# Kernel optimization log

Measured on AMD Instinct MI355X. Metric: run time of the kernel, lower is better.

The kernel has to match this reference:

```python
import jax, jax.numpy as jnp
import numpy as np

D_MODEL = 1024
N_HEADS = 16
HEAD_DIM = D_MODEL // N_HEADS
NUM_SINK = 4
WINDOW = 512
B, S = 1, 4096


def _sink_visible(S):
    # visible[i, j] = (j <= i) & ((j < NUM_SINK) | (j >= i - WINDOW + 1))
    i = jnp.arange(S)[:, None]
    j = jnp.arange(S)[None, :]
    return (j <= i) & ((j < NUM_SINK) | (j >= i - WINDOW + 1))


def setup_inputs() -> dict:
    key = jax.random.key(0)
    kx, kq, kk, kv, ko = jax.random.split(key, 5)
    sc = 1.0 / np.sqrt(D_MODEL)
    return {
        "x": jax.random.normal(kx, (B, S, D_MODEL), dtype=jnp.float32),
        "Wq": jax.random.normal(kq, (D_MODEL, D_MODEL), dtype=jnp.float32) * sc,
        "Wk": jax.random.normal(kk, (D_MODEL, D_MODEL), dtype=jnp.float32) * sc,
        "Wv": jax.random.normal(kv, (D_MODEL, D_MODEL), dtype=jnp.float32) * sc,
        "Wo": jax.random.normal(ko, (D_MODEL, D_MODEL), dtype=jnp.float32) * sc,
    }


def reference(x, Wq, Wk, Wv, Wo):
    Bx, Sx, D = x.shape
    H, hd = N_HEADS, HEAD_DIM
    # nn.Linear (no bias): y = x @ W^T
    q = (x @ Wq.T).reshape(Bx, Sx, H, hd).transpose(0, 2, 1, 3)  # (B,H,S,hd)
    k = (x @ Wk.T).reshape(Bx, Sx, H, hd).transpose(0, 2, 1, 3)
    v = (x @ Wv.T).reshape(Bx, Sx, H, hd).transpose(0, 2, 1, 3)
    scale = 1.0 / np.sqrt(hd)
    scores = jnp.einsum("bhqd,bhkd->bhqk", q, k) * scale  # (B,H,S,S)
    visible = _sink_visible(Sx)  # (S,S) bool; every row has j=i visible
    scores = jnp.where(visible[None, None], scores, -jnp.inf)
    attn = jax.nn.softmax(scores, axis=-1)
    out = jnp.einsum("bhqk,bhkd->bhqd", attn, v)
    out = out.transpose(0, 2, 1, 3).reshape(Bx, Sx, D)
    return out @ Wo.T
```

## Files before the change

### kernel.cpp

```cpp
#include <hip/hip_runtime.h>
#include <stdint.h>

#define AS1 __attribute__((address_space(1)))
#define AS3 __attribute__((address_space(3)))

typedef short short8 __attribute__((ext_vector_type(8)));
typedef unsigned short ushort8 __attribute__((ext_vector_type(8)));
typedef __bf16 bf16x8 __attribute__((ext_vector_type(8)));
typedef float floatx4 __attribute__((ext_vector_type(4)));

__device__ __forceinline__ floatx4 mfma16(short8 a, short8 b, floatx4 c) {
  return __builtin_amdgcn_mfma_f32_16x16x32_bf16(
      __builtin_bit_cast(bf16x8, a), __builtin_bit_cast(bf16x8, b), c, 0, 0, 0);
}

__device__ __forceinline__ unsigned short f2bf(float f) {
  uint32_t u = __builtin_bit_cast(uint32_t, f);
  u = (u + 0x7FFFu + ((u >> 16) & 1u)) >> 16;
  return (unsigned short)u;
}

__device__ __forceinline__ uint32_t cvt_pk_bf16(float a, float b) {
  uint32_t d;
  asm("v_cvt_pk_bf16_f32 %0, %1, %2" : "=v"(d) : "v"(a), "v"(b));
  return d;
}

__device__ __forceinline__ size_t tiled_off(int row, int col) {
  int rt = row >> 7, c8 = (row >> 4) & 7, rr = row & 15;
  int t = col >> 5, lh = (col >> 3) & 3, e = col & 7;
  return ((size_t)((rt * 32 + t) * 8 + c8) << 9) + (lh * 16 + rr) * 8 + e;
}

__global__ __launch_bounds__(256) void convert_pack(
    const float* __restrict__ x, const float* __restrict__ wq,
    const float* __restrict__ wk, const float* __restrict__ wv,
    const float* __restrict__ wo, unsigned short* __restrict__ xb,
    unsigned short* __restrict__ wqkvb, unsigned short* __restrict__ wob) {
  const int lane = threadIdx.x & 63;
  const int wid = threadIdx.x >> 6;
  const int b = blockIdx.x * 4 + wid;
  const int lrow = lane & 15, lkg = lane >> 4;
  const float* src;
  unsigned short* dst;
  if (b < 8192) {
    int rt = b >> 8, wi = b & 255, t = wi >> 3, c8 = wi & 7;
    int row = rt * 128 + c8 * 16 + lrow;
    src = x + (size_t)row * 1024 + t * 32 + lkg * 8;
    dst = xb + ((size_t)b << 9) + lane * 8;
  } else if (b < 14336) {
    int jb = b - 8192;
    int rt = jb >> 8, wi = jb & 255, t = wi >> 3, c8 = wi & 7;
    int row = rt * 128 + c8 * 16 + lrow;
    int r = row >> 10, srow = row & 1023;
    const float* m = (r == 0) ? wq : (r == 1) ? wk : wv;
    src = m + (size_t)srow * 1024 + t * 32 + lkg * 8;
    dst = wqkvb + ((size_t)jb << 9) + lane * 8;
  } else {
    int jb = b - 14336;
    int rt = jb >> 8, wi = jb & 255, t = wi >> 3, c8 = wi & 7;
    int row = rt * 128 + c8 * 16 + lrow;
    src = wo + (size_t)row * 1024 + t * 32 + lkg * 8;
    dst = wob + ((size_t)jb << 9) + lane * 8;
  }
  float4 a = *(const float4*)src;
  float4 c = *(const float4*)(src + 4);
  ushort8 o;
  o[0] = f2bf(a.x); o[1] = f2bf(a.y); o[2] = f2bf(a.z); o[3] = f2bf(a.w);
  o[4] = f2bf(c.x); o[5] = f2bf(c.y); o[6] = f2bf(c.z); o[7] = f2bf(c.w);
  *(ushort8*)dst = o;
}

template <typename OutT>
__global__ __launch_bounds__(256) void gemm_bt(const unsigned short* __restrict__ A,
                                               const unsigned short* __restrict__ Bm,
                                               OutT* __restrict__ C, int N, int K) {
  __shared__ unsigned short lds[3][16 * 512];
  const int tid = threadIdx.x;
  const int lane = tid & 63;
  const int w = tid >> 6;
  const int wr = w >> 1, wc = w & 1;

  const int lid = blockIdx.y * gridDim.x + blockIdx.x;
  const int xcd = lid & 7;
  const int wgid = xcd * 96 + (lid >> 3);
  const int s = wgid >> 5, w5 = wgid & 31;
  const int mt = (s & 3) * 8 + (w5 & 7);
  const int nt = (s >> 2) * 4 + (w5 >> 3);
  const int tm = mt * 128, tn = nt * 128;
  const int lrow = lane & 15;

  floatx4 acc[4][4];
#pragma unroll
  for (int i = 0; i < 4; ++i)
#pragma unroll
    for (int j = 0; j < 4; ++j) acc[i][j] = floatx4{0.f, 0.f, 0.f, 0.f};

  auto stage = [&](unsigned short* buf, int t) {
#pragma unroll
    for (int c = w * 4; c < w * 4 + 4; ++c) {
      const unsigned short* g;
      if (c < 8)
        g = A + ((size_t)((mt * 32 + t) * 8 + c) << 9) + lane * 8;
      else
        g = Bm + ((size_t)((nt * 32 + t) * 8 + (c - 8)) << 9) + lane * 8;
      __builtin_amdgcn_global_load_lds((const AS1 uint32_t*)g,
                                       (AS3 uint32_t*)(buf + c * 512), 16, 0, 0);
    }
  };

  auto compute = [&](const unsigned short* L) {
    short8 af[4], bf[4];
#pragma unroll
    for (int i = 0; i < 4; ++i)
      af[i] = *(const short8*)&L[(wr * 4 + i) * 512 + lane * 8];
#pragma unroll
    for (int j = 0; j < 4; ++j)
      bf[j] = *(const short8*)&L[(8 + wc * 4 + j) * 512 + lane * 8];
#pragma unroll
    for (int i = 0; i < 4; ++i)
#pragma unroll
      for (int j = 0; j < 4; ++j) acc[i][j] = mfma16(af[i], bf[j], acc[i][j]);
  };

  stage(lds[0], 0);
  stage(lds[1], 1);

  const int T = K >> 5;
  int bt = 0;
  for (int t = 0; t < T - 1; ++t) {
    asm volatile("s_waitcnt vmcnt(4)" ::: "memory");
    __builtin_amdgcn_sched_barrier(0);
    __builtin_amdgcn_s_barrier();
    __builtin_amdgcn_sched_barrier(0);
    if (t + 2 < T) {
      int b2 = (bt + 2 >= 3) ? bt - 1 : bt + 2;
      stage(lds[b2], t + 2);
    }
    compute(lds[bt]);
    bt = (bt + 1 == 3) ? 0 : bt + 1;
  }
  asm volatile("s_waitcnt vmcnt(0)" ::: "memory");
  __builtin_amdgcn_sched_barrier(0);
  __builtin_amdgcn_s_barrier();
  __builtin_amdgcn_sched_barrier(0);
  compute(lds[bt]);

  const int r0 = (lane >> 4) * 4;
#pragma unroll
  for (int i = 0; i < 4; ++i)
#pragma unroll
    for (int j = 0; j < 4; ++j)
#pragma unroll
      for (int r = 0; r < 4; ++r) {
        int row = tm + wr * 64 + i * 16 + r0 + r;
        int col = tn + wc * 64 + j * 16 + lrow;
        float v = acc[i][j][r];
        if constexpr (sizeof(OutT) == 2)
          C[(size_t)row * N + col] = f2bf(v);
        else
          C[(size_t)row * N + col] = v;
      }
}

__global__ __launch_bounds__(256) void gemm64(const unsigned short* __restrict__ A,
                                              const unsigned short* __restrict__ Bm,
                                              float* __restrict__ C, int N, int K) {
  __shared__ unsigned short lds[3][12 * 512];
  const int tid = threadIdx.x;
  const int lane = tid & 63;
  const int w = tid >> 6;
  const int wr = w >> 1, wc = w & 1;

  const int lid = blockIdx.y * gridDim.x + blockIdx.x;
  const int xcd = lid & 7;
  const int wgid = xcd * 64 + (lid >> 3);
  const int s = wgid >> 5, w5 = wgid & 31;
  const int mt = (s & 3) * 16 + (w5 & 15);
  const int nt = (s >> 2) * 2 + (w5 >> 4);
  const int tm = mt * 64, tn = nt * 128;
  const int lrow = lane & 15;

  floatx4 acc[2][4];
#pragma unroll
  for (int i = 0; i < 2; ++i)
#pragma unroll
    for (int j = 0; j < 4; ++j) acc[i][j] = floatx4{0.f, 0.f, 0.f, 0.f};

  auto stage = [&](unsigned short* buf, int t) {
#pragma unroll
    for (int c = w * 3; c < w * 3 + 3; ++c) {
      const unsigned short* g;
      if (c < 4)
        g = A + ((size_t)(((mt >> 1) * 32 + t) * 8 + ((mt & 1) * 4 + c)) << 9) + lane * 8;
      else
        g = Bm + ((size_t)((nt * 32 + t) * 8 + (c - 4)) << 9) + lane * 8;
      __builtin_amdgcn_global_load_lds((const AS1 uint32_t*)g,
                                       (AS3 uint32_t*)(buf + c * 512), 16, 0, 0);
    }
  };

  auto compute = [&](const unsigned short* L) {
    short8 af[2], bf[4];
#pragma unroll
    for (int i = 0; i < 2; ++i)
      af[i] = *(const short8*)&L[(wr * 2 + i) * 512 + lane * 8];
#pragma unroll
    for (int j = 0; j < 4; ++j)
      bf[j] = *(const short8*)&L[(4 + wc * 4 + j) * 512 + lane * 8];
#pragma unroll
    for (int i = 0; i < 2; ++i)
#pragma unroll
      for (int j = 0; j < 4; ++j) acc[i][j] = mfma16(af[i], bf[j], acc[i][j]);
  };

  stage(lds[0], 0);
  stage(lds[1], 1);

  const int T = K >> 5;
  int bt = 0;
  for (int t = 0; t < T - 1; ++t) {
    asm volatile("s_waitcnt vmcnt(3)" ::: "memory");
    __builtin_amdgcn_sched_barrier(0);
    __builtin_amdgcn_s_barrier();
    __builtin_amdgcn_sched_barrier(0);
    if (t + 2 < T) {
      int b2 = (bt + 2 >= 3) ? bt - 1 : bt + 2;
      stage(lds[b2], t + 2);
    }
    compute(lds[bt]);
    bt = (bt + 1 == 3) ? 0 : bt + 1;
  }
  asm volatile("s_waitcnt vmcnt(0)" ::: "memory");
  __builtin_amdgcn_sched_barrier(0);
  __builtin_amdgcn_s_barrier();
  __builtin_amdgcn_sched_barrier(0);
  compute(lds[bt]);

  const int r0 = (lane >> 4) * 4;
#pragma unroll
  for (int i = 0; i < 2; ++i)
#pragma unroll
    for (int j = 0; j < 4; ++j)
#pragma unroll
      for (int r = 0; r < 4; ++r) {
        int row = tm + (wr * 2 + i) * 16 + r0 + r;
        int col = tn + (wc * 4 + j) * 16 + lrow;
        C[(size_t)row * N + col] = acc[i][j][r];
      }
}

__global__ __launch_bounds__(256) void attn_kernel(const unsigned short* __restrict__ qkv,
                                                   unsigned short* __restrict__ aout) {
  __shared__ unsigned short Klds[2][16 * 512];
  __shared__ unsigned short VT[64 * 136];
  __shared__ unsigned short PT[4][16 * 136];

  const int tid = threadIdx.x;
  const int lane = tid & 63;
  const int w = tid >> 6;
  const int lrow = lane & 15;
  const int lkg = lane >> 4;

  const int i = blockIdx.x;
  const int half = i >> 8;
  const int j = (i >> 3) & 31;
  const int h = 2 * (i & 7) + half;
  const int qb = half ? (31 - j) : j;
  const int q0 = qb * 128;

  short8 qf[2][2];
#pragma unroll
  for (int qt = 0; qt < 2; ++qt)
#pragma unroll
    for (int ks = 0; ks < 2; ++ks)
      qf[qt][ks] = *(const short8*)&qkv[(size_t)(q0 + qt * 64 + w * 16 + lrow) * 3072 +
                                        h * 64 + ks * 32 + lkg * 8];

  float m_i[2], l_i[2];
  floatx4 o[4][2];
#pragma unroll
  for (int qt = 0; qt < 2; ++qt) {
    m_i[qt] = -1e30f;
    l_i[qt] = 0.f;
#pragma unroll
    for (int nt = 0; nt < 4; ++nt) o[nt][qt] = floatx4{0.f, 0.f, 0.f, 0.f};
  }

  const float scale2 = 0.125f * 1.44269504088896f;

  if (w < 2) {
    const unsigned short* g = &qkv[(size_t)lrow * 3072 + 1024 + h * 64 + w * 32 + lkg * 8];
    __builtin_amdgcn_global_load_lds((const AS1 uint32_t*)g,
                                     (AS3 uint32_t*)(&Klds[0][w * 512]), 16, 0, 0);
  }
  {
    if (lane < 16) {
      const unsigned short* g0 = &qkv[(size_t)(2 * lane) * 3072 + 2048 + h * 64 + w * 16];
      ushort8 a0 = *(const ushort8*)g0;
      ushort8 a1 = *(const ushort8*)(g0 + 8);
      ushort8 b0 = *(const ushort8*)(g0 + 3072);
      ushort8 b1 = *(const ushort8*)(g0 + 3080);
      uint32_t* vt = (uint32_t*)VT;
#pragma unroll
      for (int dd = 0; dd < 8; ++dd) {
        vt[(w * 16 + dd) * 68 + lane] = (uint32_t)a0[dd] | ((uint32_t)b0[dd] << 16);
        vt[(w * 16 + 8 + dd) * 68 + lane] = (uint32_t)a1[dd] | ((uint32_t)b1[dd] << 16);
      }
    }
  }
  const int kb0 = (q0 - 511 < 16) ? 16 : (q0 - 511);
#pragma unroll
  for (int c = 0; c < 4; ++c) {
    int ch = w * 4 + c;
    int kt = ch >> 1, ks = ch & 1;
    const unsigned short* g =
        &qkv[(size_t)(kb0 + kt * 16 + lrow) * 3072 + 1024 + h * 64 + ks * 32 + lkg * 8];
    __builtin_amdgcn_global_load_lds((const AS1 uint32_t*)g,
                                     (AS3 uint32_t*)(&Klds[1][ch * 512]), 16, 0, 0);
  }
  ushort8 va0, va1, vb0, vb1;
  {
    const unsigned short* g0 = &qkv[(size_t)(kb0 + 2 * lane) * 3072 + 2048 + h * 64 + w * 16];
    va0 = *(const ushort8*)g0;
    va1 = *(const ushort8*)(g0 + 8);
    vb0 = *(const ushort8*)(g0 + 3072);
    vb1 = *(const ushort8*)(g0 + 3080);
  }
  __syncthreads();

#pragma unroll
  for (int qt = 0; qt < 2; ++qt) {
    const int qq = q0 + qt * 64 + w * 16 + lrow;
    floatx4 s0 = floatx4{0.f, 0.f, 0.f, 0.f};
#pragma unroll
    for (int ks = 0; ks < 2; ++ks) {
      short8 kf = *(const short8*)&Klds[0][ks * 512 + lane * 8];
      s0 = mfma16(kf, qf[qt][ks], s0);
    }
    float mx = -1e30f;
    float sv[4];
#pragma unroll
    for (int r = 0; r < 4; ++r) {
      int key = lkg * 4 + r;
      bool vis = (key <= qq) && ((key < 4) || (key >= qq - 511));
      sv[r] = vis ? s0[r] * scale2 : -1e30f;
      mx = fmaxf(mx, sv[r]);
    }
    mx = fmaxf(mx, __shfl_xor(mx, 16));
    mx = fmaxf(mx, __shfl_xor(mx, 32));
    m_i[qt] = mx;
    float p0 = exp2f(sv[0] - mx), p1 = exp2f(sv[1] - mx);
    float p2 = exp2f(sv[2] - mx), p3 = exp2f(sv[3] - mx);
    float ps = (p0 + p1) + (p2 + p3);
    *(uint2*)&PT[w][lrow * 136 + lkg * 4] = uint2{cvt_pk_bf16(p0, p1), cvt_pk_bf16(p2, p3)};
    *(uint2*)&PT[w][lrow * 136 + 16 + lkg * 4] = uint2{0u, 0u};
    ps += __shfl_xor(ps, 16);
    ps += __shfl_xor(ps, 32);
    l_i[qt] = ps;
    short8 pf = *(const short8*)&PT[w][lrow * 136 + lkg * 8];
#pragma unroll
    for (int nt = 0; nt < 4; ++nt) {
      short8 vf = *(const short8*)&VT[(nt * 16 + lrow) * 136 + lkg * 8];
      o[nt][qt] = mfma16(vf, pf, o[nt][qt]);
    }
  }

  int nbuf = 1;
  for (int kb = kb0; kb < q0 + 128; kb += 128) {
    const bool hasnext = (kb + 128 < q0 + 128);
    __syncthreads();
    {
      uint32_t* vt = (uint32_t*)VT;
#pragma unroll
      for (int dd = 0; dd < 8; ++dd) {
        vt[(w * 16 + dd) * 68 + lane] = (uint32_t)va0[dd] | ((uint32_t)vb0[dd] << 16);
        vt[(w * 16 + 8 + dd) * 68 + lane] = (uint32_t)va1[dd] | ((uint32_t)vb1[dd] << 16);
      }
    }
    __syncthreads();

    if (hasnext) {
      const int kn = kb + 128;
#pragma unroll
      for (int c = 0; c < 4; ++c) {
        int ch = w * 4 + c;
        int kt = ch >> 1, ks = ch & 1;
        const unsigned short* g =
            &qkv[(size_t)(kn + kt * 16 + lrow) * 3072 + 1024 + h * 64 + ks * 32 + lkg * 8];
        __builtin_amdgcn_global_load_lds((const AS1 uint32_t*)g,
                                         (AS3 uint32_t*)(&Klds[1 - nbuf][ch * 512]), 16, 0, 0);
      }
      const unsigned short* g0 = &qkv[(size_t)(kn + 2 * lane) * 3072 + 2048 + h * 64 + w * 16];
      va0 = *(const ushort8*)g0;
      va1 = *(const ushort8*)(g0 + 8);
      vb0 = *(const ushort8*)(g0 + 3072);
      vb1 = *(const ushort8*)(g0 + 3080);
    }

#pragma unroll
    for (int qt = 0; qt < 2; ++qt) {
      const int qaT = q0 + qt * 64 + w * 16;
      const int qq = qaT + lrow;
      floatx4 s[8];
#pragma unroll
      for (int ct = 0; ct < 8; ++ct) {
        s[ct] = floatx4{0.f, 0.f, 0.f, 0.f};
#pragma unroll
        for (int ks = 0; ks < 2; ++ks) {
          short8 kf = *(const short8*)&Klds[nbuf][(ct * 2 + ks) * 512 + lane * 8];
          s[ct] = mfma16(kf, qf[qt][ks], s[ct]);
        }
      }
      const bool full = (kb + 127 <= qaT) && (kb >= qaT + 15 - 511);
      float mx = -1e30f;
#pragma unroll
      for (int ct = 0; ct < 8; ++ct)
#pragma unroll
        for (int r = 0; r < 4; ++r) {
          float val = s[ct][r] * scale2;
          if (!full) {
            int key = kb + ct * 16 + lkg * 4 + r;
            bool vis = (key <= qq) && (key >= qq - 511);
            val = vis ? val : -1e30f;
          }
          s[ct][r] = val;
          mx = fmaxf(mx, val);
        }
      mx = fmaxf(mx, __shfl_xor(mx, 16));
      mx = fmaxf(mx, __shfl_xor(mx, 32));
      float nm = fmaxf(m_i[qt], mx);
      float alpha = exp2f(m_i[qt] - nm);
      m_i[qt] = nm;

      float ps = 0.f;
#pragma unroll
      for (int ct = 0; ct < 8; ++ct) {
        float p0 = exp2f(s[ct][0] - nm), p1 = exp2f(s[ct][1] - nm);
        float p2 = exp2f(s[ct][2] - nm), p3 = exp2f(s[ct][3] - nm);
        ps += (p0 + p1) + (p2 + p3);
        *(uint2*)&PT[w][lrow * 136 + ct * 16 + lkg * 4] =
            uint2{cvt_pk_bf16(p0, p1), cvt_pk_bf16(p2, p3)};
      }
      ps += __shfl_xor(ps, 16);
      ps += __shfl_xor(ps, 32);
      l_i[qt] = l_i[qt] * alpha + ps;

#pragma unroll
      for (int nt = 0; nt < 4; ++nt)
#pragma unroll
        for (int r = 0; r < 4; ++r) o[nt][qt][r] *= alpha;

#pragma unroll
      for (int kk = 0; kk < 4; ++kk) {
        short8 pf = *(const short8*)&PT[w][lrow * 136 + kk * 32 + lkg * 8];
#pragma unroll
        for (int nt = 0; nt < 4; ++nt) {
          short8 vf = *(const short8*)&VT[(nt * 16 + lrow) * 136 + kk * 32 + lkg * 8];
          o[nt][qt] = mfma16(vf, pf, o[nt][qt]);
        }
      }
    }
    nbuf ^= 1;
  }

#pragma unroll
  for (int qt = 0; qt < 2; ++qt) {
    const int qq = q0 + qt * 64 + w * 16 + lrow;
    const float inv = 1.0f / l_i[qt];
#pragma unroll
    for (int nt = 0; nt < 4; ++nt) {
      floatx4 ov = o[nt][qt];
      uint32_t lo = cvt_pk_bf16(ov[0] * inv, ov[1] * inv);
      uint32_t hi = cvt_pk_bf16(ov[2] * inv, ov[3] * inv);
      int col = h * 64 + nt * 16 + lkg * 4;
      *(uint2*)&aout[tiled_off(qq, col)] = uint2{lo, hi};
    }
  }
}

extern "C" void kernel_launch(void* const* d_in, const int* in_sizes, int n_in,
                              void* d_out, int out_size, void* d_ws, size_t ws_size,
                              hipStream_t stream) {
  const float* x = (const float*)d_in[0];
  const float* wq = (const float*)d_in[1];
  const float* wk = (const float*)d_in[2];
  const float* wv = (const float*)d_in[3];
  const float* wo = (const float*)d_in[4];

  char* ws = (char*)d_ws;
  unsigned short* Xb = (unsigned short*)(ws);
  unsigned short* Wqkv = (unsigned short*)(ws + (8u << 20));
  unsigned short* Wob = (unsigned short*)(ws + (14u << 20));
  unsigned short* QKV = (unsigned short*)(ws + (16u << 20));
  unsigned short* AO = (unsigned short*)(ws + (40u << 20));

  convert_pack<<<4096, 256, 0, stream>>>(x, wq, wk, wv, wo, Xb, Wqkv, Wob);
  gemm_bt<unsigned short><<<dim3(32, 24), 256, 0, stream>>>(Xb, Wqkv, QKV, 3072, 1024);
  attn_kernel<<<512, 256, 0, stream>>>(QKV, AO);
  gemm64<<<dim3(64, 8), 256, 0, stream>>>(AO, Wob, (float*)d_out, 1024, 1024);
}
```

Measured before the change: 161.3 us.

## Enlarge QKV GEMM tiles to 256x256 with eight waves per block

The QKV projection GEMM now uses 256x256 output tiles computed by 512-thread blocks of eight waves, each wave owning a 128x64 sub-tile. LDS staging doubles to cover the larger A and B panels, and the block-to-tile swizzle is rewritten for the 16x12 grid. The aim is higher arithmetic intensity per global/LDS load. The risk is that only 192 blocks run on a 256-CU device, with higher register pressure from the 8x4 accumulator array.

```diff
diff --git a/kernel.cpp b/kernel.cpp
--- a/kernel.cpp
+++ b/kernel.cpp
@@ -72,27 +72,27 @@
 }
 
 template <typename OutT>
-__global__ __launch_bounds__(256) void gemm_bt(const unsigned short* __restrict__ A,
+__global__ __launch_bounds__(512) void gemm_bt(const unsigned short* __restrict__ A,
                                                const unsigned short* __restrict__ Bm,
                                                OutT* __restrict__ C, int N, int K) {
-  __shared__ unsigned short lds[3][16 * 512];
+  __shared__ unsigned short lds[3][32 * 512];
   const int tid = threadIdx.x;
   const int lane = tid & 63;
   const int w = tid >> 6;
-  const int wr = w >> 1, wc = w & 1;
+  const int wrm = w >> 2;
+  const int wcn = w & 3;
+  const int lrow = lane & 15;
 
   const int lid = blockIdx.y * gridDim.x + blockIdx.x;
   const int xcd = lid & 7;
-  const int wgid = xcd * 96 + (lid >> 3);
-  const int s = wgid >> 5, w5 = wgid & 31;
-  const int mt = (s & 3) * 8 + (w5 & 7);
-  const int nt = (s >> 2) * 4 + (w5 >> 3);
-  const int tm = mt * 128, tn = nt * 128;
-  const int lrow = lane & 15;
-
-  floatx4 acc[4][4];
-#pragma unroll
-  for (int i = 0; i < 4; ++i)
+  const int idx = lid >> 3;
+  const int mt = (xcd & 3) * 4 + (idx & 3);
+  const int nt = (xcd >> 2) * 6 + (idx >> 2);
+  const int tm = mt * 256, tn = nt * 256;
+
+  floatx4 acc[8][4];
+#pragma unroll
+  for (int i = 0; i < 8; ++i)
 #pragma unroll
     for (int j = 0; j < 4; ++j) acc[i][j] = floatx4{0.f, 0.f, 0.f, 0.f};
 
@@ -100,25 +100,29 @@
 #pragma unroll
     for (int c = w * 4; c < w * 4 + 4; ++c) {
       const unsigned short* g;
-      if (c < 8)
-        g = A + ((size_t)((mt * 32 + t) * 8 + c) << 9) + lane * 8;
-      else
-        g = Bm + ((size_t)((nt * 32 + t) * 8 + (c - 8)) << 9) + lane * 8;
+      if (c < 16) {
+        int rt = 2 * mt + (c >> 3);
+        g = A + ((size_t)((rt * 32 + t) * 8 + (c & 7)) << 9) + lane * 8;
+      } else {
+        int cc = c - 16;
+        int rt = 2 * nt + (cc >> 3);
+        g = Bm + ((size_t)((rt * 32 + t) * 8 + (cc & 7)) << 9) + lane * 8;
+      }
       __builtin_amdgcn_global_load_lds((const AS1 uint32_t*)g,
                                        (AS3 uint32_t*)(buf + c * 512), 16, 0, 0);
     }
   };
 
   auto compute = [&](const unsigned short* L) {
-    short8 af[4], bf[4];
-#pragma unroll
-    for (int i = 0; i < 4; ++i)
-      af[i] = *(const short8*)&L[(wr * 4 + i) * 512 + lane * 8];
+    short8 af[8], bf[4];
+#pragma unroll
+    for (int i = 0; i < 8; ++i)
+      af[i] = *(const short8*)&L[(wrm * 8 + i) * 512 + lane * 8];
 #pragma unroll
     for (int j = 0; j < 4; ++j)
-      bf[j] = *(const short8*)&L[(8 + wc * 4 + j) * 512 + lane * 8];
-#pragma unroll
-    for (int i = 0; i < 4; ++i)
+      bf[j] = *(const short8*)&L[(16 + wcn * 4 + j) * 512 + lane * 8];
+#pragma unroll
+    for (int i = 0; i < 8; ++i)
 #pragma unroll
       for (int j = 0; j < 4; ++j) acc[i][j] = mfma16(af[i], bf[j], acc[i][j]);
   };
@@ -148,13 +152,13 @@
 
   const int r0 = (lane >> 4) * 4;
 #pragma unroll
-  for (int i = 0; i < 4; ++i)
+  for (int i = 0; i < 8; ++i)
 #pragma unroll
     for (int j = 0; j < 4; ++j)
 #pragma unroll
       for (int r = 0; r < 4; ++r) {
-        int row = tm + wr * 64 + i * 16 + r0 + r;
-        int col = tn + wc * 64 + j * 16 + lrow;
+        int row = tm + wrm * 128 + i * 16 + r0 + r;
+        int col = tn + wcn * 64 + j * 16 + lrow;
         float v = acc[i][j][r];
         if constexpr (sizeof(OutT) == 2)
           C[(size_t)row * N + col] = f2bf(v);
@@ -496,7 +500,7 @@
   unsigned short* AO = (unsigned short*)(ws + (40u << 20));
 
   convert_pack<<<4096, 256, 0, stream>>>(x, wq, wk, wv, wo, Xb, Wqkv, Wob);
-  gemm_bt<unsigned short><<<dim3(32, 24), 256, 0, stream>>>(Xb, Wqkv, QKV, 3072, 1024);
+  gemm_bt<unsigned short><<<dim3(16, 12), 512, 0, stream>>>(Xb, Wqkv, QKV, 3072, 1024);
   attn_kernel<<<512, 256, 0, stream>>>(QKV, AO);
   gemm64<<<dim3(64, 8), 256, 0, stream>>>(AO, Wob, (float*)d_out, 1024, 1024);
 }
```

Result: slower. 167.7 us (+4.0%).

## Write Q/K in MFMA-tiled per-head layout and V head-major from QKV GEMM

Applied to the files above, without the earlier changes.

The QKV projection epilogue now scatters Q and K into a per-head, MFMA-fragment-tiled layout and V into a head-major contiguous layout, in place of one interleaved row-major QKV buffer. The attention kernel reads Q fragments, K tiles (via global_load_lds) and V rows as contiguous 1KB chunks instead of strided rows with a 3072-element pitch. This targets the uncoalesced loads in attention. The cost is scattered 2-byte stores in the GEMM epilogue. The K window start also shifts from q0-511 to q0-512, which aligns the block to 16 rows for the tiled indexing.

```diff
diff --git a/kernel.cpp b/kernel.cpp
--- a/kernel.cpp
+++ b/kernel.cpp
@@ -30,6 +30,11 @@
   int rt = row >> 7, c8 = (row >> 4) & 7, rr = row & 15;
   int t = col >> 5, lh = (col >> 3) & 3, e = col & 7;
   return ((size_t)((rt * 32 + t) * 8 + c8) << 9) + (lh * 16 + rr) * 8 + e;
+}
+
+__device__ __forceinline__ size_t qk_off(int h, int row, int dd) {
+  return ((size_t)((h * 256 + (row >> 4)) * 2 + (dd >> 5)) << 9) +
+         ((((dd >> 3) & 3) * 16 + (row & 15)) << 3) + (dd & 7);
 }
 
 __global__ __launch_bounds__(256) void convert_pack(
@@ -71,10 +76,12 @@
   *(ushort8*)dst = o;
 }
 
-template <typename OutT>
-__global__ __launch_bounds__(256) void gemm_bt(const unsigned short* __restrict__ A,
-                                               const unsigned short* __restrict__ Bm,
-                                               OutT* __restrict__ C, int N, int K) {
+__global__ __launch_bounds__(256) void gemm_qkv(const unsigned short* __restrict__ A,
+                                                const unsigned short* __restrict__ Bm,
+                                                unsigned short* __restrict__ Qb,
+                                                unsigned short* __restrict__ Kb,
+                                                unsigned short* __restrict__ Vh,
+                                                int K) {
   __shared__ unsigned short lds[3][16 * 512];
   const int tid = threadIdx.x;
   const int lane = tid & 63;
@@ -146,6 +153,7 @@
   __builtin_amdgcn_sched_barrier(0);
   compute(lds[bt]);
 
+  const int which = tn >> 10;
   const int r0 = (lane >> 4) * 4;
 #pragma unroll
   for (int i = 0; i < 4; ++i)
@@ -155,11 +163,14 @@
       for (int r = 0; r < 4; ++r) {
         int row = tm + wr * 64 + i * 16 + r0 + r;
         int col = tn + wc * 64 + j * 16 + lrow;
-        float v = acc[i][j][r];
-        if constexpr (sizeof(OutT) == 2)
-          C[(size_t)row * N + col] = f2bf(v);
+        int h = (col >> 6) & 15, dd = col & 63;
+        unsigned short v = f2bf(acc[i][j][r]);
+        if (which == 0)
+          Qb[qk_off(h, row, dd)] = v;
+        else if (which == 1)
+          Kb[qk_off(h, row, dd)] = v;
         else
-          C[(size_t)row * N + col] = v;
+          Vh[((size_t)h * 4096 + row) * 64 + dd] = v;
       }
 }
 
@@ -250,7 +261,9 @@
       }
 }
 
-__global__ __launch_bounds__(256) void attn_kernel(const unsigned short* __restrict__ qkv,
+__global__ __launch_bounds__(256) void attn_kernel(const unsigned short* __restrict__ Qb,
+                                                   const unsigned short* __restrict__ Kb,
+                                                   const unsigned short* __restrict__ Vh,
                                                    unsigned short* __restrict__ aout) {
   __shared__ unsigned short Klds[2][16 * 512];
   __shared__ unsigned short VT[64 * 136];
@@ -274,8 +287,8 @@
   for (int qt = 0; qt < 2; ++qt)
 #pragma unroll
     for (int ks = 0; ks < 2; ++ks)
-      qf[qt][ks] = *(const short8*)&qkv[(size_t)(q0 + qt * 64 + w * 16 + lrow) * 3072 +
-                                        h * 64 + ks * 32 + lkg * 8];
+      qf[qt][ks] = *(const short8*)&Qb[((size_t)((h * 256 + (q0 >> 4) + qt * 4 + w) * 2 + ks)
+                                        << 9) + lane * 8];
 
   float m_i[2], l_i[2];
   floatx4 o[4][2];
@@ -290,17 +303,17 @@
   const float scale2 = 0.125f * 1.44269504088896f;
 
   if (w < 2) {
-    const unsigned short* g = &qkv[(size_t)lrow * 3072 + 1024 + h * 64 + w * 32 + lkg * 8];
+    const unsigned short* g = Kb + ((size_t)((h * 256 + 0) * 2 + w) << 9) + lane * 8;
     __builtin_amdgcn_global_load_lds((const AS1 uint32_t*)g,
                                      (AS3 uint32_t*)(&Klds[0][w * 512]), 16, 0, 0);
   }
   {
     if (lane < 16) {
-      const unsigned short* g0 = &qkv[(size_t)(2 * lane) * 3072 + 2048 + h * 64 + w * 16];
+      const unsigned short* g0 = Vh + ((size_t)h * 4096 + 2 * lane) * 64 + w * 16;
       ushort8 a0 = *(const ushort8*)g0;
       ushort8 a1 = *(const ushort8*)(g0 + 8);
-      ushort8 b0 = *(const ushort8*)(g0 + 3072);
-      ushort8 b1 = *(const ushort8*)(g0 + 3080);
+      ushort8 b0 = *(const ushort8*)(g0 + 64);
+      ushort8 b1 = *(const ushort8*)(g0 + 72);
       uint32_t* vt = (uint32_t*)VT;
 #pragma unroll
       for (int dd = 0; dd < 8; ++dd) {
@@ -309,23 +322,23 @@
       }
     }
   }
-  const int kb0 = (q0 - 511 < 16) ? 16 : (q0 - 511);
+  const int kb0 = (q0 - 512 < 16) ? 16 : (q0 - 512);
 #pragma unroll
   for (int c = 0; c < 4; ++c) {
     int ch = w * 4 + c;
     int kt = ch >> 1, ks = ch & 1;
     const unsigned short* g =
-        &qkv[(size_t)(kb0 + kt * 16 + lrow) * 3072 + 1024 + h * 64 + ks * 32 + lkg * 8];
+        Kb + ((size_t)((h * 256 + (kb0 >> 4) + kt) * 2 + ks) << 9) + lane * 8;
     __builtin_amdgcn_global_load_lds((const AS1 uint32_t*)g,
                                      (AS3 uint32_t*)(&Klds[1][ch * 512]), 16, 0, 0);
   }
   ushort8 va0, va1, vb0, vb1;
   {
-    const unsigned short* g0 = &qkv[(size_t)(kb0 + 2 * lane) * 3072 + 2048 + h * 64 + w * 16];
+    const unsigned short* g0 = Vh + ((size_t)h * 4096 + kb0 + 2 * lane) * 64 + w * 16;
     va0 = *(const ushort8*)g0;
     va1 = *(const ushort8*)(g0 + 8);
-    vb0 = *(const ushort8*)(g0 + 3072);
-    vb1 = *(const ushort8*)(g0 + 3080);
+    vb0 = *(const ushort8*)(g0 + 64);
+    vb1 = *(const ushort8*)(g0 + 72);
   }
   __syncthreads();
 
@@ -387,15 +400,15 @@
         int ch = w * 4 + c;
         int kt = ch >> 1, ks = ch & 1;
         const unsigned short* g =
-            &qkv[(size_t)(kn + kt * 16 + lrow) * 3072 + 1024 + h * 64 + ks * 32 + lkg * 8];
+            Kb + ((size_t)((h * 256 + (kn >> 4) + kt) * 2 + ks) << 9) + lane * 8;
         __builtin_amdgcn_global_load_lds((const AS1 uint32_t*)g,
                                          (AS3 uint32_t*)(&Klds[1 - nbuf][ch * 512]), 16, 0, 0);
       }
-      const unsigned short* g0 = &qkv[(size_t)(kn + 2 * lane) * 3072 + 2048 + h * 64 + w * 16];
+      const unsigned short* g0 = Vh + ((size_t)h * 4096 + kn + 2 * lane) * 64 + w * 16;
       va0 = *(const ushort8*)g0;
       va1 = *(const ushort8*)(g0 + 8);
-      vb0 = *(const ushort8*)(g0 + 3072);
-      vb1 = *(const ushort8*)(g0 + 3080);
+      vb0 = *(const ushort8*)(g0 + 64);
+      vb1 = *(const ushort8*)(g0 + 72);
     }
 
 #pragma unroll
@@ -492,11 +505,13 @@
   unsigned short* Xb = (unsigned short*)(ws);
   unsigned short* Wqkv = (unsigned short*)(ws + (8u << 20));
   unsigned short* Wob = (unsigned short*)(ws + (14u << 20));
-  unsigned short* QKV = (unsigned short*)(ws + (16u << 20));
+  unsigned short* Qb = (unsigned short*)(ws + (16u << 20));
+  unsigned short* Kb = (unsigned short*)(ws + (24u << 20));
+  unsigned short* Vh = (unsigned short*)(ws + (32u << 20));
   unsigned short* AO = (unsigned short*)(ws + (40u << 20));
 
   convert_pack<<<4096, 256, 0, stream>>>(x, wq, wk, wv, wo, Xb, Wqkv, Wob);
-  gemm_bt<unsigned short><<<dim3(32, 24), 256, 0, stream>>>(Xb, Wqkv, QKV, 3072, 1024);
-  attn_kernel<<<512, 256, 0, stream>>>(QKV, AO);
+  gemm_qkv<<<dim3(32, 24), 256, 0, stream>>>(Xb, Wqkv, Qb, Kb, Vh, 1024);
+  attn_kernel<<<512, 256, 0, stream>>>(Qb, Kb, Vh, AO);
   gemm64<<<dim3(64, 8), 256, 0, stream>>>(AO, Wob, (float*)d_out, 1024, 1024);
 }
```

After: 165.9 us. +2.9%, slower.
